# Performance work log

Measured on AMD Instinct MI355X. Metric: run time of the kernel, lower is better.

## Reference

```python
import jax, jax.numpy as jnp
import numpy as np

NUM_RBF = 16
TOP_K = 30
LOWER = 0.0
UPPER = 20.0
MAX_REL = 32  # PositionalEncodings max_relative_feature


def layer_norm(x, g, b, eps=1e-5):
    m = jnp.mean(x, -1, keepdims=True)
    v = jnp.var(x, -1, keepdims=True)
    return (x - m) / jnp.sqrt(v + eps) * g + b


def rbf(D):
    # exp(-((D - mu)/sigma)^2), mu = linspace(LOWER, UPPER, NUM_RBF)
    mu = jnp.linspace(LOWER, UPPER, NUM_RBF)
    sigma = (UPPER - LOWER) / NUM_RBF
    return jnp.exp(-(((D[..., None] - mu) / sigma) ** 2))


def setup_inputs() -> dict:
    key = jax.random.key(0)
    ks = jax.random.split(key, 6)
    B, L, A = 1, 1536, 14
    x = jax.random.normal(ks[0], (B, L, A, 3), jnp.float32) * 5.0
    S = jax.random.randint(ks[1], (B, L), 0, 21)
    mask = jnp.ones((B, L), jnp.float32)
    atom14_mask = jnp.ones((B, L, A), jnp.float32)
    R_idx = jnp.broadcast_to(jnp.arange(L, dtype=jnp.int32), (B, L))
    chain_labels = jnp.zeros((B, L), jnp.int32)
    protein_mpnn_feat = jax.random.normal(ks[2], (B, L, 128), jnp.float32)
    W_pos = jax.random.normal(ks[3], (2 * MAX_REL + 2, 16), jnp.float32) * 0.12
    b_pos = jnp.zeros((16,), jnp.float32)
    W_edge = jax.random.normal(ks[4], (16 + NUM_RBF * 14 * 14, 128), jnp.float32) * 0.018
    gamma_e = jnp.ones((128,), jnp.float32)
    beta_e = jnp.zeros((128,), jnp.float32)
    W_node = jax.random.normal(ks[5], (21 + 128, 128), jnp.float32) * 0.08
    gamma_n = jnp.ones((128,), jnp.float32)
    beta_n = jnp.zeros((128,), jnp.float32)
    return dict(x=x, mask=mask, atom14_mask=atom14_mask,
                protein_mpnn_feat=protein_mpnn_feat,
                W_pos=W_pos, b_pos=b_pos, W_edge=W_edge, gamma_e=gamma_e,
                beta_e=beta_e, W_node=W_node, gamma_n=gamma_n, beta_n=beta_n,
                S=S, R_idx=R_idx, chain_labels=chain_labels)


def reference(x, mask, atom14_mask, protein_mpnn_feat,
              W_pos, b_pos, W_edge, gamma_e, beta_e,
              W_node, gamma_n, beta_n, S, R_idx, chain_labels):
    B, L, A, _ = x.shape  # A = 14
    X_m = atom14_mask * mask[:, :, None]          # [B,L,14]
    Ca = x[:, :, 1]                                # CA_idx = 1

    # ---- _dist: masked pairwise CA distances + kNN topk (smallest) ----
    m2 = mask[:, None, :] * mask[:, :, None]       # [B,L,L]
    dX = Ca[:, None, :, :] - Ca[:, :, None, :]
    D = m2 * jnp.sqrt(jnp.sum(dX ** 2, -1) + 1e-6)
    D_max = jnp.max(D, -1, keepdims=True)
    D_adjust = D + (1.0 - m2) * D_max
    _, E_idx = jax.lax.top_k(-D_adjust, TOP_K)     # [B,L,K] smallest distances

    bidx = jnp.arange(B)[:, None, None]
    # gather neighbor atom coords / masks (all_coords_list == x in atom14 order)
    Xg = x[bidx, E_idx]                            # [B,L,K,14,3]
    Xm_g = X_m[bidx, E_idx]                        # [B,L,K,14]

    # ---- 14x14 pairwise atom RBFs to neighbors, fused/vectorized ----
    # Dp[b,l,k,i,j] = ||x[b,l,i] - x[b,E_idx[b,l,k],j]||
    Dp = jnp.sqrt(jnp.sum((x[:, :, None, :, None, :] - Xg[:, :, :, None, :, :]) ** 2, -1) + 1e-6)
    R = rbf(Dp)                                    # [B,L,K,14,14,16]
    R = R * X_m[:, :, None, :, None, None] * Xm_g[:, :, :, None, :, None]
    # torch loop cats atom_1-major, atom_2, then rbf bins -> same as reshape
    RBF_all = R.reshape(B, L, TOP_K, A * A * NUM_RBF)  # [B,L,K,3136]

    # ---- positional encodings ----
    offset = R_idx[:, :, None] - R_idx[:, None, :]           # [B,L,L]
    offset_g = jnp.take_along_axis(offset, E_idx, axis=2)    # [B,L,K]
    d_chains = (chain_labels[:, :, None] == chain_labels[:, None, :]).astype(jnp.int32)
    E_chains = jnp.take_along_axis(d_chains, E_idx, axis=2)  # [B,L,K]
    d = jnp.clip(offset_g + MAX_REL, 0, 2 * MAX_REL) * E_chains \
        + (1 - E_chains) * (2 * MAX_REL + 1)
    E_pos = jax.nn.one_hot(d, 2 * MAX_REL + 2, dtype=x.dtype) @ W_pos + b_pos

    # ---- edge embedding ----
    E = jnp.concatenate([E_pos, RBF_all], -1) @ W_edge       # [B,L,K,128]
    E = layer_norm(E, gamma_e, beta_e)

    # ---- node embedding ----
    V = jnp.concatenate([jax.nn.one_hot(S, 21, dtype=x.dtype), protein_mpnn_feat], -1) @ W_node
    V = layer_norm(V, gamma_n, beta_n)

    return (V, E, E_idx, x)
```

## Files before the change

### kernel.cpp

```cpp
#include <hip/hip_runtime.h>
#include <hip/hip_bf16.h>
#include <hip/hip_fp16.h>
#include <math.h>

#define LL 1536
#define NA 14
#define TOPK 30
#define KDIM 3152
#define KPAD 3200
#define NCHUNK 50

#define TOPK_BLKS 384
#define CONV_BLKS 100
#define NODE_BLKS 384
#define PREP_BLKS (TOPK_BLKS + CONV_BLKS + NODE_BLKS)

#define EDGE_BLKS 768

typedef __attribute__((ext_vector_type(8))) short bf16x8;
typedef __attribute__((ext_vector_type(4))) float f32x4;

static __device__ __forceinline__ ushort f2bf(float f) {
    union { __hip_bfloat16 h; ushort u; } v;
    v.h = __float2bfloat16(f);
    return v.u;
}

static __device__ __forceinline__ float fexp2(float f) {
    return __builtin_amdgcn_exp2f(f);
}

static __device__ __forceinline__ unsigned cvt_pk_bf16(float lo, float hi) {
    unsigned r;
    asm("v_cvt_pk_bf16_f32 %0, %1, %2" : "=v"(r) : "v"(lo), "v"(hi));
    return r;
}

static __device__ __forceinline__ unsigned long long u64min(
    unsigned long long a, unsigned long long b) { return a < b ? a : b; }

#define ASYNC16(ldsp, gp)                                                     \
    __builtin_amdgcn_global_load_lds(                                         \
        (const __attribute__((address_space(1))) void*)(gp),                  \
        (__attribute__((address_space(3))) void*)(ldsp), 16, 0, 0)

__global__ __launch_bounds__(256) void prep_kernel(
    const float* __restrict__ x, const float* __restrict__ mask,
    const float* __restrict__ feat,
    const float* __restrict__ W_edge, ushort* __restrict__ Wt,
    const float* __restrict__ W_node, const float* __restrict__ gamma_n,
    const float* __restrict__ beta_n, const int* __restrict__ S,
    float* __restrict__ V, float* __restrict__ out_idx, float* __restrict__ out_x)
{
    __shared__ __align__(16) char sm[24576];
    const int blk = blockIdx.x;
    const int tid = threadIdx.x;

    if (blk < TOPK_BLKS) {
        float* ca  = (float*)sm;
        float* msk = (float*)sm + 4608;
        for (int t = tid; t < LL; t += 256) {
            msk[t] = mask[t];
            ca[t * 3 + 0] = x[t * 42 + 3];
            ca[t * 3 + 1] = x[t * 42 + 4];
            ca[t * 3 + 2] = x[t * 42 + 5];
        }
        __syncthreads();

        const int lane = tid & 63;
        const int i = blk * 4 + (tid >> 6);
        const float cix = ca[i * 3 + 0], ciy = ca[i * 3 + 1], ciz = ca[i * 3 + 2];
        const float mi = msk[i];

        float d[24], m2a[24];
        float lmax = 0.f;
        #pragma unroll
        for (int c = 0; c < 24; ++c) {
            int j = lane + c * 64;
            float dx = ca[j * 3 + 0] - cix;
            float dy = ca[j * 3 + 1] - ciy;
            float dz = ca[j * 3 + 2] - ciz;
            float m2 = mi * msk[j];
            float D = m2 * sqrtf(dx * dx + dy * dy + dz * dz + 1e-6f);
            d[c] = D; m2a[c] = m2;
            lmax = fmaxf(lmax, D);
        }
        #pragma unroll
        for (int m = 1; m < 64; m <<= 1) lmax = fmaxf(lmax, __shfl_xor(lmax, m));

        unsigned long long key[24];
        #pragma unroll
        for (int c = 0; c < 24; ++c) {
            float adj = d[c] + (1.f - m2a[c]) * lmax;
            key[c] = ((unsigned long long)__float_as_uint(adj) << 32)
                   | (unsigned)(lane + c * 64);
        }
        for (int t = 0; t < TOPK; ++t) {
            unsigned long long m12[12];
            #pragma unroll
            for (int c = 0; c < 12; ++c) m12[c] = u64min(key[2 * c], key[2 * c + 1]);
            #pragma unroll
            for (int c = 0; c < 6; ++c) m12[c] = u64min(m12[2 * c], m12[2 * c + 1]);
            unsigned long long best = u64min(u64min(m12[0], m12[1]),
                u64min(m12[2], u64min(m12[3], u64min(m12[4], m12[5]))));
            #pragma unroll
            for (int m = 1; m < 64; m <<= 1) best = u64min(best, __shfl_xor(best, m));
            if (lane == 0) out_idx[i * TOPK + t] = (float)(unsigned)(best & 0xffffffffu);
            #pragma unroll
            for (int c = 0; c < 24; ++c) if (key[c] == best) key[c] = ~0ull;
        }
        for (int t = lane; t < 42; t += 64) out_x[i * 42 + t] = x[i * 42 + t];

    } else if (blk < TOPK_BLKS + CONV_BLKS) {
        int cb = blk - TOPK_BLKS;
        int k0 = (cb % 50) * 64, n0 = (cb / 50) * 64;
        float (*tile)[65] = (float (*)[65])sm;
        #pragma unroll
        for (int r = 0; r < 16; ++r) {
            int idx = r * 256 + tid;
            int kl = idx >> 6, nl = idx & 63;
            int k = k0 + kl;
            tile[nl][kl] = (k < KDIM) ? W_edge[k * 128 + n0 + nl] : 0.f;
        }
        __syncthreads();
        #pragma unroll
        for (int r = 0; r < 8; ++r) {
            int idx = r * 256 + tid;
            int nl = idx >> 5, kp = (idx & 31) * 2;
            unsigned pk = cvt_pk_bf16(tile[nl][kp], tile[nl][kp + 1]);
            *(unsigned*)&Wt[(size_t)(n0 + nl) * KPAD + k0 + kp] = pk;
        }

    } else {
        int nb = blk - TOPK_BLKS - CONV_BLKS;
        float* f = (float*)sm;
        const int w = tid >> 6, lane = tid & 63;
        const int i = nb * 4 + w;
        f[w * 128 + lane] = feat[i * 128 + lane];
        f[w * 128 + 64 + lane] = feat[i * 128 + 64 + lane];
        __syncthreads();
        int s = S[i];
        float a0 = W_node[s * 128 + lane];
        float a1 = W_node[s * 128 + 64 + lane];
        #pragma unroll 8
        for (int c = 0; c < 128; ++c) {
            float fc = f[w * 128 + c];
            a0 = fmaf(fc, W_node[(21 + c) * 128 + lane], a0);
            a1 = fmaf(fc, W_node[(21 + c) * 128 + 64 + lane], a1);
        }
        float ss = a0 + a1, qq = a0 * a0 + a1 * a1;
        #pragma unroll
        for (int m = 1; m < 64; m <<= 1) {
            ss += __shfl_xor(ss, m);
            qq += __shfl_xor(qq, m);
        }
        float mean = ss * (1.f / 128.f);
        float var = qq * (1.f / 128.f) - mean * mean;
        float inv = 1.f / sqrtf(var + 1e-5f);
        V[i * 128 + lane]      = (a0 - mean) * inv * gamma_n[lane] + beta_n[lane];
        V[i * 128 + 64 + lane] = (a1 - mean) * inv * gamma_n[64 + lane] + beta_n[64 + lane];
    }
}

__global__ __launch_bounds__(256, 3) void edge_mfma_kernel(
    const float* __restrict__ x, const float* __restrict__ mask,
    const float* __restrict__ a14m, const float* __restrict__ W_pos,
    const float* __restrict__ b_pos, const ushort* __restrict__ Wt,
    const float* __restrict__ gamma, const float* __restrict__ beta,
    const int* __restrict__ R_idx, const int* __restrict__ chain,
    const float* __restrict__ idxf, float* __restrict__ E)
{
    __shared__ __align__(16) char arena[45824];
    ushort* Bs    = (ushort*)arena;
    __half* ddc   = (__half*)(arena + 16384);
    ushort* eposs = (ushort*)(arena + 41984);
    int*    jl    = (int*)(arena + 44032);
    float*  lnS   = (float*)(arena + 44288);
    float*  lnQ   = (float*)(arena + 44800);
    float*  xi    = (float*)(arena + 45312);
    float*  mi    = (float*)(arena + 45664);

    const int i0 = blockIdx.x * 2;
    const int tid = threadIdx.x;
    const int wave = tid >> 6, lane = tid & 63;

    if (tid < 64) {
        int g = tid >> 5, e = tid & 31;
        jl[tid] = (e < TOPK) ? (int)idxf[(i0 + g) * TOPK + e] : 0;
    } else if (tid < 64 + 84) {
        int t = tid - 64; int g = t / 42, c = t - g * 42;
        xi[g * 44 + c] = x[(i0 + g) * 42 + c];
    } else if (tid < 148 + 28) {
        int t = tid - 148; int g = t / 14, a = t - g * 14;
        mi[g * 16 + a] = a14m[(i0 + g) * 14 + a] * mask[i0 + g];
    }
    __syncthreads();

    const int srow = wave * 32 + (lane >> 3);
    const int sseg = (lane & 7) ^ ((lane >> 3) & 7);
    const ushort* gsrc = Wt + (size_t)srow * KPAD + sseg * 8;
    #pragma unroll
    for (int it = 0; it < 4; ++it)
        ASYNC16(Bs + wave * 2048 + it * 512, gsrc + (size_t)it * 8 * KPAD);

    for (int t = tid; t < 64 * 16; t += 256) {
        int row = t >> 4, c = t & 15;
        int e = row & 31, g = row >> 5;
        float v = 0.f;
        if (e < TOPK) {
            int i = i0 + g, j = jl[row];
            int off = R_idx[i] - R_idx[j];
            int ec = (chain[i] == chain[j]) ? 1 : 0;
            int dc = off + 32; dc = dc < 0 ? 0 : (dc > 64 ? 64 : dc);
            int d = ec ? dc : 65;
            v = W_pos[d * 16 + c] + b_pos[c];
        }
        eposs[row * 16 + c] = f2bf(v);
    }

    for (int t = tid; t < 64 * 196; t += 256) {
        int row = t / 196, p = t - row * 196;
        int a1 = p / 14, a2 = p - a1 * 14;
        int g = row >> 5, e = row & 31;
        int j = jl[row];
        const float* xj = &x[j * 42 + a2 * 3];
        float dx = xi[g * 44 + a1 * 3 + 0] - xj[0];
        float dy = xi[g * 44 + a1 * 3 + 1] - xj[1];
        float dz = xi[g * 44 + a1 * 3 + 2] - xj[2];
        float dd = sqrtf(dx * dx + dy * dy + dz * dz + 1e-6f);
        float cj_ = (e < TOPK) ? a14m[j * 14 + a2] * mask[j] : 0.f;
        float coef = mi[g * 16 + a1] * cj_;
        ddc[row * 200 + p] = __float2half((coef > 0.5f) ? fminf(dd, 27.f) : 40.f);
    }
    __syncthreads();

    const int l16 = lane & 15, lk = lane >> 4;
    const int mh = wave >> 1, nh = wave & 1;
    const int r0 = 8 * (lk & 1);
    const float mu0 = (float)r0 * 1.33333333f;
    float wc[7];
    #pragma unroll
    for (int j = 1; j < 8; ++j)
        wc[j - 1] = __expf(-1.13777778f * (float)(2 * (r0 + j) - 1));

    int boff[2][4];
    #pragma unroll
    for (int ks = 0; ks < 2; ++ks)
        #pragma unroll
        for (int nf = 0; nf < 4; ++nf) {
            int n = nh * 64 + nf * 16 + l16;
            boff[ks][nf] = n * 64 + ((((ks << 2) | lk) ^ (n & 7)) << 3);
        }
    int doff[2], eoff[2];
    #pragma unroll
    for (int mf = 0; mf < 2; ++mf) {
        int row = mh * 32 + mf * 16 + l16;
        doff[mf] = row * 200;
        eoff[mf] = row * 16 + r0;
    }

    f32x4 acc[2][4] = {};

    for (int ch = 0; ch < NCHUNK; ++ch) {
        bf16x8 bfr[2][4];
        #pragma unroll
        for (int ks = 0; ks < 2; ++ks)
            #pragma unroll
            for (int nf = 0; nf < 4; ++nf)
                bfr[ks][nf] = *(const bf16x8*)&Bs[boff[ks][nf]];
        __syncthreads();
        if (ch + 1 < NCHUNK) {
            #pragma unroll
            for (int it = 0; it < 4; ++it)
                ASYNC16(Bs + wave * 2048 + it * 512,
                        gsrc + (size_t)it * 8 * KPAD + (ch + 1) * 64);
        }
        bf16x8 af[2][2];
        #pragma unroll
        for (int ks = 0; ks < 2; ++ks) {
            const int p = 4 * ch + 2 * ks + (lk >> 1) - 1;
            #pragma unroll
            for (int mf = 0; mf < 2; ++mf) {
                if (p < 0) {
                    af[ks][mf] = *(const bf16x8*)&eposs[eoff[mf]];
                } else if (p < 196) {
                    float dd = __half2float(ddc[doff[mf] + p]);
                    float w = fexp2(dd * 2.46219921f);
                    float s = dd - mu0;
                    float ev[8];
                    ev[0] = fexp2(s * s * -0.92332483f);
                    #pragma unroll
                    for (int j = 1; j < 8; ++j) ev[j] = ev[j - 1] * w * wc[j - 1];
                    union { unsigned u[4]; bf16x8 v; } o;
                    #pragma unroll
                    for (int j = 0; j < 4; ++j)
                        o.u[j] = cvt_pk_bf16(ev[2 * j], ev[2 * j + 1]);
                    af[ks][mf] = o.v;
                } else {
                    af[ks][mf] = (bf16x8){0, 0, 0, 0, 0, 0, 0, 0};
                }
            }
        }
        #pragma unroll
        for (int ks = 0; ks < 2; ++ks)
            #pragma unroll
            for (int mf = 0; mf < 2; ++mf)
                #pragma unroll
                for (int nf = 0; nf < 4; ++nf)
                    acc[mf][nf] = __builtin_amdgcn_mfma_f32_16x16x32_bf16(
                        af[ks][mf], bfr[ks][nf], acc[mf][nf], 0, 0, 0);
        __syncthreads();
    }

    #pragma unroll
    for (int mf = 0; mf < 2; ++mf)
        #pragma unroll
        for (int reg = 0; reg < 4; ++reg) {
            float s = acc[mf][0][reg] + acc[mf][1][reg] + acc[mf][2][reg] + acc[mf][3][reg];
            float q = acc[mf][0][reg] * acc[mf][0][reg] + acc[mf][1][reg] * acc[mf][1][reg]
                    + acc[mf][2][reg] * acc[mf][2][reg] + acc[mf][3][reg] * acc[mf][3][reg];
            #pragma unroll
            for (int m = 1; m < 16; m <<= 1) {
                s += __shfl_xor(s, m);
                q += __shfl_xor(q, m);
            }
            if (l16 == 0) {
                int row = mh * 32 + mf * 16 + lk * 4 + reg;
                lnS[row * 2 + nh] = s;
                lnQ[row * 2 + nh] = q;
            }
        }
    __syncthreads();

    float gl[4], bl[4];
    #pragma unroll
    for (int nf = 0; nf < 4; ++nf) {
        int col = nh * 64 + nf * 16 + l16;
        gl[nf] = gamma[col];
        bl[nf] = beta[col];
    }
    #pragma unroll
    for (int mf = 0; mf < 2; ++mf)
        #pragma unroll
        for (int reg = 0; reg < 4; ++reg) {
            int r = mh * 32 + mf * 16 + lk * 4 + reg;
            int e = r & 31, g = r >> 5;
            if (e < TOPK) {
                float s = lnS[r * 2 + 0] + lnS[r * 2 + 1];
                float q = lnQ[r * 2 + 0] + lnQ[r * 2 + 1];
                float mean = s * (1.f / 128.f);
                float var = q * (1.f / 128.f) - mean * mean;
                float inv = 1.f / sqrtf(var + 1e-5f);
                float* dst = &E[((size_t)((i0 + g) * TOPK + e)) * 128];
                #pragma unroll
                for (int nf = 0; nf < 4; ++nf) {
                    int col = nh * 64 + nf * 16 + l16;
                    dst[col] = (acc[mf][nf][reg] - mean) * inv * gl[nf] + bl[nf];
                }
            }
        }
}

extern "C" void kernel_launch(void* const* d_in, const int* in_sizes, int n_in,
                              void* d_out, int out_size, void* d_ws, size_t ws_size,
                              hipStream_t stream)
{
    const float* x       = (const float*)d_in[0];
    const float* mask    = (const float*)d_in[1];
    const float* a14m    = (const float*)d_in[2];
    const float* feat    = (const float*)d_in[3];
    const float* W_pos   = (const float*)d_in[4];
    const float* b_pos   = (const float*)d_in[5];
    const float* W_edge  = (const float*)d_in[6];
    const float* gamma_e = (const float*)d_in[7];
    const float* beta_e  = (const float*)d_in[8];
    const float* W_node  = (const float*)d_in[9];
    const float* gamma_n = (const float*)d_in[10];
    const float* beta_n  = (const float*)d_in[11];
    const int*   S       = (const int*)d_in[12];
    const int*   R_idx   = (const int*)d_in[13];
    const int*   chain   = (const int*)d_in[14];

    float* out     = (float*)d_out;
    float* V       = out;
    float* E       = out + 196608;
    float* out_idx = out + 196608 + 5898240;
    float* out_x   = out_idx + 46080;

    ushort* Wt = (ushort*)d_ws;

    prep_kernel<<<PREP_BLKS, 256, 0, stream>>>(
        x, mask, feat, W_edge, Wt, W_node, gamma_n, beta_n, S, V, out_idx, out_x);
    edge_mfma_kernel<<<EDGE_BLKS, 256, 0, stream>>>(
        x, mask, a14m, W_pos, b_pos, Wt, gamma_e, beta_e, R_idx, chain,
        out_idx, E);
}
```

Measured before the change: 121.3 us.

## Restructure edge GEMM: LDS double-buffered RBF A-tiles, register-prefetched W from global

```diff
diff --git a/kernel.cpp b/kernel.cpp
--- a/kernel.cpp
+++ b/kernel.cpp
@@ -20,12 +20,6 @@
 typedef __attribute__((ext_vector_type(8))) short bf16x8;
 typedef __attribute__((ext_vector_type(4))) float f32x4;
 
-static __device__ __forceinline__ ushort f2bf(float f) {
-    union { __hip_bfloat16 h; ushort u; } v;
-    v.h = __float2bfloat16(f);
-    return v.u;
-}
-
 static __device__ __forceinline__ float fexp2(float f) {
     return __builtin_amdgcn_exp2f(f);
 }
@@ -39,10 +33,30 @@
 static __device__ __forceinline__ unsigned long long u64min(
     unsigned long long a, unsigned long long b) { return a < b ? a : b; }
 
-#define ASYNC16(ldsp, gp)                                                     \
-    __builtin_amdgcn_global_load_lds(                                         \
-        (const __attribute__((address_space(1))) void*)(gp),                  \
-        (__attribute__((address_space(3))) void*)(ldsp), 16, 0, 0)
+static __device__ __forceinline__ void build_rbf(
+    ushort* dst, float4 xi4, float4 xj4,
+    const float (&cA)[7], const float (&cB)[7])
+{
+    float dx = xi4.x - xj4.x, dy = xi4.y - xj4.y, dz = xi4.z - xj4.z;
+    float dd = sqrtf(dx * dx + dy * dy + dz * dz + 1e-6f);
+    dd = fminf(dd, 27.f);
+    float coef = xi4.w * xj4.w;
+    float w = fexp2(dd * 2.46219921f);
+    float ev[16];
+    float s8 = dd - 10.66666667f;
+    ev[0] = fexp2(-0.92332483f * dd * dd) * coef;
+    ev[8] = fexp2(-0.92332483f * s8 * s8) * coef;
+    #pragma unroll
+    for (int j = 1; j <= 7; ++j) {
+        ev[j]     = ev[j - 1]     * w * cA[j - 1];
+        ev[8 + j] = ev[8 + j - 1] * w * cB[j - 1];
+    }
+    union { unsigned u[8]; uint4 q[2]; } o;
+    #pragma unroll
+    for (int c = 0; c < 8; ++c) o.u[c] = cvt_pk_bf16(ev[2 * c], ev[2 * c + 1]);
+    *(uint4*)&dst[0] = o.q[0];
+    *(uint4*)&dst[8] = o.q[1];
+}
 
 __global__ __launch_bounds__(256) void prep_kernel(
     const float* __restrict__ x, const float* __restrict__ mask,
@@ -170,15 +184,12 @@
     const int* __restrict__ R_idx, const int* __restrict__ chain,
     const float* __restrict__ idxf, float* __restrict__ E)
 {
-    __shared__ __align__(16) char arena[45824];
-    ushort* Bs    = (ushort*)arena;
-    __half* ddc   = (__half*)(arena + 16384);
-    ushort* eposs = (ushort*)(arena + 41984);
-    int*    jl    = (int*)(arena + 44032);
-    float*  lnS   = (float*)(arena + 44288);
-    float*  lnQ   = (float*)(arena + 44800);
-    float*  xi    = (float*)(arena + 45312);
-    float*  mi    = (float*)(arena + 45664);
+    __shared__ __align__(16) ushort As[2][64][72];
+    __shared__ __align__(16) float4 xjr[64][14];
+    __shared__ __align__(16) float4 xir[2][14];
+    __shared__ int   jl[64];
+    __shared__ float lnS[64][2];
+    __shared__ float lnQ[64][2];
 
     const int i0 = blockIdx.x * 2;
     const int tid = threadIdx.x;
@@ -187,130 +198,130 @@
     if (tid < 64) {
         int g = tid >> 5, e = tid & 31;
         jl[tid] = (e < TOPK) ? (int)idxf[(i0 + g) * TOPK + e] : 0;
-    } else if (tid < 64 + 84) {
-        int t = tid - 64; int g = t / 42, c = t - g * 42;
-        xi[g * 44 + c] = x[(i0 + g) * 42 + c];
-    } else if (tid < 148 + 28) {
-        int t = tid - 148; int g = t / 14, a = t - g * 14;
-        mi[g * 16 + a] = a14m[(i0 + g) * 14 + a] * mask[i0 + g];
+    } else if (tid < 64 + 28) {
+        int t = tid - 64, g = t / 14, a = t - g * 14;
+        const float* xp = &x[(i0 + g) * 42 + a * 3];
+        xir[g][a] = make_float4(xp[0], xp[1], xp[2],
+                                a14m[(i0 + g) * 14 + a] * mask[i0 + g]);
     }
     __syncthreads();
 
-    const int srow = wave * 32 + (lane >> 3);
-    const int sseg = (lane & 7) ^ ((lane >> 3) & 7);
-    const ushort* gsrc = Wt + (size_t)srow * KPAD + sseg * 8;
-    #pragma unroll
-    for (int it = 0; it < 4; ++it)
-        ASYNC16(Bs + wave * 2048 + it * 512, gsrc + (size_t)it * 8 * KPAD);
-
-    for (int t = tid; t < 64 * 16; t += 256) {
-        int row = t >> 4, c = t & 15;
-        int e = row & 31, g = row >> 5;
-        float v = 0.f;
-        if (e < TOPK) {
-            int i = i0 + g, j = jl[row];
+    for (int t = tid; t < 64 * 14; t += 256) {
+        int row = t / 14, a = t - row * 14;
+        int e = row & 31, j = jl[row];
+        const float* xp = &x[j * 42 + a * 3];
+        float mj = (e < TOPK) ? a14m[j * 14 + a] * mask[j] : 0.f;
+        xjr[row][a] = make_float4(xp[0], xp[1], xp[2], mj);
+    }
+    __syncthreads();
+
+    const int l16 = lane & 15, lk = lane >> 4, lk8 = lk * 8;
+    const int mh = wave >> 1, nh = wave & 1;
+    const int arow0 = mh * 32 + l16, arow1 = arow0 + 16;
+    const int row_b = tid >> 2, slot = tid & 3;
+    const int gb = row_b >> 5, eb = row_b & 31;
+
+    float cA[7], cB[7];
+    #pragma unroll
+    for (int j = 1; j <= 7; ++j) {
+        cA[j - 1] = __expf(-1.13777778f * (float)(2 * j - 1));
+        cB[j - 1] = __expf(-1.13777778f * (float)(2 * (j + 8) - 1));
+    }
+
+    if (slot == 0) {
+        float v[16];
+        if (eb < TOPK) {
+            int i = i0 + gb, j = jl[row_b];
             int off = R_idx[i] - R_idx[j];
             int ec = (chain[i] == chain[j]) ? 1 : 0;
             int dc = off + 32; dc = dc < 0 ? 0 : (dc > 64 ? 64 : dc);
             int d = ec ? dc : 65;
-            v = W_pos[d * 16 + c] + b_pos[c];
-        }
-        eposs[row * 16 + c] = f2bf(v);
-    }
-
-    for (int t = tid; t < 64 * 196; t += 256) {
-        int row = t / 196, p = t - row * 196;
-        int a1 = p / 14, a2 = p - a1 * 14;
-        int g = row >> 5, e = row & 31;
-        int j = jl[row];
-        const float* xj = &x[j * 42 + a2 * 3];
-        float dx = xi[g * 44 + a1 * 3 + 0] - xj[0];
-        float dy = xi[g * 44 + a1 * 3 + 1] - xj[1];
-        float dz = xi[g * 44 + a1 * 3 + 2] - xj[2];
-        float dd = sqrtf(dx * dx + dy * dy + dz * dz + 1e-6f);
-        float cj_ = (e < TOPK) ? a14m[j * 14 + a2] * mask[j] : 0.f;
-        float coef = mi[g * 16 + a1] * cj_;
-        ddc[row * 200 + p] = __float2half((coef > 0.5f) ? fminf(dd, 27.f) : 40.f);
-    }
+            #pragma unroll
+            for (int c = 0; c < 16; ++c) v[c] = W_pos[d * 16 + c] + b_pos[c];
+        } else {
+            #pragma unroll
+            for (int c = 0; c < 16; ++c) v[c] = 0.f;
+        }
+        union { unsigned u[8]; uint4 q[2]; } o;
+        #pragma unroll
+        for (int c = 0; c < 8; ++c) o.u[c] = cvt_pk_bf16(v[2 * c], v[2 * c + 1]);
+        *(uint4*)&As[0][row_b][0] = o.q[0];
+        *(uint4*)&As[0][row_b][8] = o.q[1];
+    } else {
+        build_rbf(&As[0][row_b][slot * 16], xir[gb][slot - 1],
+                  xjr[row_b][slot - 1], cA, cB);
+    }
+
+    const ushort* bp0 = Wt + (size_t)(nh * 64 +  0 + l16) * KPAD + lk8;
+    const ushort* bp1 = Wt + (size_t)(nh * 64 + 16 + l16) * KPAD + lk8;
+    const ushort* bp2 = Wt + (size_t)(nh * 64 + 32 + l16) * KPAD + lk8;
+    const ushort* bp3 = Wt + (size_t)(nh * 64 + 48 + l16) * KPAD + lk8;
+
+    bf16x8 Ba[2][4], Bb[2][4];
+    Ba[0][0] = *(const bf16x8*)(bp0);      Ba[1][0] = *(const bf16x8*)(bp0 + 32);
+    Ba[0][1] = *(const bf16x8*)(bp1);      Ba[1][1] = *(const bf16x8*)(bp1 + 32);
+    Ba[0][2] = *(const bf16x8*)(bp2);      Ba[1][2] = *(const bf16x8*)(bp2 + 32);
+    Ba[0][3] = *(const bf16x8*)(bp3);      Ba[1][3] = *(const bf16x8*)(bp3 + 32);
+
+    int p = slot + 3, a1 = 0, a2 = slot + 3;
+    f32x4 acc[2][4] = {};
+
     __syncthreads();
 
-    const int l16 = lane & 15, lk = lane >> 4;
-    const int mh = wave >> 1, nh = wave & 1;
-    const int r0 = 8 * (lk & 1);
-    const float mu0 = (float)r0 * 1.33333333f;
-    float wc[7];
-    #pragma unroll
-    for (int j = 1; j < 8; ++j)
-        wc[j - 1] = __expf(-1.13777778f * (float)(2 * (r0 + j) - 1));
-
-    int boff[2][4];
-    #pragma unroll
-    for (int ks = 0; ks < 2; ++ks)
-        #pragma unroll
-        for (int nf = 0; nf < 4; ++nf) {
-            int n = nh * 64 + nf * 16 + l16;
-            boff[ks][nf] = n * 64 + ((((ks << 2) | lk) ^ (n & 7)) << 3);
-        }
-    int doff[2], eoff[2];
-    #pragma unroll
-    for (int mf = 0; mf < 2; ++mf) {
-        int row = mh * 32 + mf * 16 + l16;
-        doff[mf] = row * 200;
-        eoff[mf] = row * 16 + r0;
-    }
-
-    f32x4 acc[2][4] = {};
-
-    for (int ch = 0; ch < NCHUNK; ++ch) {
-        bf16x8 bfr[2][4];
-        #pragma unroll
-        for (int ks = 0; ks < 2; ++ks)
-            #pragma unroll
-            for (int nf = 0; nf < 4; ++nf)
-                bfr[ks][nf] = *(const bf16x8*)&Bs[boff[ks][nf]];
-        __syncthreads();
-        if (ch + 1 < NCHUNK) {
-            #pragma unroll
-            for (int it = 0; it < 4; ++it)
-                ASYNC16(Bs + wave * 2048 + it * 512,
-                        gsrc + (size_t)it * 8 * KPAD + (ch + 1) * 64);
-        }
-        bf16x8 af[2][2];
-        #pragma unroll
-        for (int ks = 0; ks < 2; ++ks) {
-            const int p = 4 * ch + 2 * ks + (lk >> 1) - 1;
-            #pragma unroll
-            for (int mf = 0; mf < 2; ++mf) {
-                if (p < 0) {
-                    af[ks][mf] = *(const bf16x8*)&eposs[eoff[mf]];
-                } else if (p < 196) {
-                    float dd = __half2float(ddc[doff[mf] + p]);
-                    float w = fexp2(dd * 2.46219921f);
-                    float s = dd - mu0;
-                    float ev[8];
-                    ev[0] = fexp2(s * s * -0.92332483f);
-                    #pragma unroll
-                    for (int j = 1; j < 8; ++j) ev[j] = ev[j - 1] * w * wc[j - 1];
-                    union { unsigned u[4]; bf16x8 v; } o;
-                    #pragma unroll
-                    for (int j = 0; j < 4; ++j)
-                        o.u[j] = cvt_pk_bf16(ev[2 * j], ev[2 * j + 1]);
-                    af[ks][mf] = o.v;
-                } else {
-                    af[ks][mf] = (bf16x8){0, 0, 0, 0, 0, 0, 0, 0};
-                }
-            }
-        }
-        #pragma unroll
-        for (int ks = 0; ks < 2; ++ks)
-            #pragma unroll
-            for (int mf = 0; mf < 2; ++mf)
-                #pragma unroll
-                for (int nf = 0; nf < 4; ++nf)
-                    acc[mf][nf] = __builtin_amdgcn_mfma_f32_16x16x32_bf16(
-                        af[ks][mf], bfr[ks][nf], acc[mf][nf], 0, 0, 0);
-        __syncthreads();
-    }
+#define STEP(CH, RD, BC, BN)                                                   \
+    do {                                                                       \
+        if ((CH) + 1 < NCHUNK) {                                               \
+            const size_t koff = (size_t)((CH) + 1) * 64;                       \
+            BN[0][0] = *(const bf16x8*)(bp0 + koff);                           \
+            BN[1][0] = *(const bf16x8*)(bp0 + koff + 32);                      \
+            BN[0][1] = *(const bf16x8*)(bp1 + koff);                           \
+            BN[1][1] = *(const bf16x8*)(bp1 + koff + 32);                      \
+            BN[0][2] = *(const bf16x8*)(bp2 + koff);                           \
+            BN[1][2] = *(const bf16x8*)(bp2 + koff + 32);                      \
+            BN[0][3] = *(const bf16x8*)(bp3 + koff);                           \
+            BN[1][3] = *(const bf16x8*)(bp3 + koff + 32);                      \
+        }                                                                      \
+        {                                                                      \
+            bf16x8 af0k0 = *(const bf16x8*)&As[RD][arow0][lk8];                \
+            bf16x8 af1k0 = *(const bf16x8*)&As[RD][arow1][lk8];                \
+            bf16x8 af0k1 = *(const bf16x8*)&As[RD][arow0][32 + lk8];           \
+            bf16x8 af1k1 = *(const bf16x8*)&As[RD][arow1][32 + lk8];           \
+            acc[0][0] = __builtin_amdgcn_mfma_f32_16x16x32_bf16(af0k0, BC[0][0], acc[0][0], 0, 0, 0); \
+            acc[0][1] = __builtin_amdgcn_mfma_f32_16x16x32_bf16(af0k0, BC[0][1], acc[0][1], 0, 0, 0); \
+            acc[0][2] = __builtin_amdgcn_mfma_f32_16x16x32_bf16(af0k0, BC[0][2], acc[0][2], 0, 0, 0); \
+            acc[0][3] = __builtin_amdgcn_mfma_f32_16x16x32_bf16(af0k0, BC[0][3], acc[0][3], 0, 0, 0); \
+            acc[1][0] = __builtin_amdgcn_mfma_f32_16x16x32_bf16(af1k0, BC[0][0], acc[1][0], 0, 0, 0); \
+            acc[1][1] = __builtin_amdgcn_mfma_f32_16x16x32_bf16(af1k0, BC[0][1], acc[1][1], 0, 0, 0); \
+            acc[1][2] = __builtin_amdgcn_mfma_f32_16x16x32_bf16(af1k0, BC[0][2], acc[1][2], 0, 0, 0); \
+            acc[1][3] = __builtin_amdgcn_mfma_f32_16x16x32_bf16(af1k0, BC[0][3], acc[1][3], 0, 0, 0); \
+            acc[0][0] = __builtin_amdgcn_mfma_f32_16x16x32_bf16(af0k1, BC[1][0], acc[0][0], 0, 0, 0); \
+            acc[0][1] = __builtin_amdgcn_mfma_f32_16x16x32_bf16(af0k1, BC[1][1], acc[0][1], 0, 0, 0); \
+            acc[0][2] = __builtin_amdgcn_mfma_f32_16x16x32_bf16(af0k1, BC[1][2], acc[0][2], 0, 0, 0); \
+            acc[0][3] = __builtin_amdgcn_mfma_f32_16x16x32_bf16(af0k1, BC[1][3], acc[0][3], 0, 0, 0); \
+            acc[1][0] = __builtin_amdgcn_mfma_f32_16x16x32_bf16(af1k1, BC[1][0], acc[1][0], 0, 0, 0); \
+            acc[1][1] = __builtin_amdgcn_mfma_f32_16x16x32_bf16(af1k1, BC[1][1], acc[1][1], 0, 0, 0); \
+            acc[1][2] = __builtin_amdgcn_mfma_f32_16x16x32_bf16(af1k1, BC[1][2], acc[1][2], 0, 0, 0); \
+            acc[1][3] = __builtin_amdgcn_mfma_f32_16x16x32_bf16(af1k1, BC[1][3], acc[1][3], 0, 0, 0); \
+        }                                                                      \
+        if ((CH) < NCHUNK - 1) {                                               \
+            if (p <= 195) {                                                    \
+                build_rbf(&As[1 - (RD)][row_b][slot * 16], xir[gb][a1],        \
+                          xjr[row_b][a2], cA, cB);                             \
+            } else {                                                           \
+                uint4 z = {0u, 0u, 0u, 0u};                                    \
+                *(uint4*)&As[1 - (RD)][row_b][slot * 16] = z;                  \
+                *(uint4*)&As[1 - (RD)][row_b][slot * 16 + 8] = z;              \
+            }                                                                  \
+            p += 4; a2 += 4; if (a2 >= 14) { a2 -= 14; ++a1; }                 \
+        }                                                                      \
+        __syncthreads();                                                       \
+    } while (0)
+
+    for (int ch = 0; ch < NCHUNK; ch += 2) {
+        STEP(ch, 0, Ba, Bb);
+        STEP(ch + 1, 1, Bb, Ba);
+    }
+#undef STEP
 
     #pragma unroll
     for (int mf = 0; mf < 2; ++mf)
@@ -326,8 +337,8 @@
             }
             if (l16 == 0) {
                 int row = mh * 32 + mf * 16 + lk * 4 + reg;
-                lnS[row * 2 + nh] = s;
-                lnQ[row * 2 + nh] = q;
+                lnS[row][nh] = s;
+                lnQ[row][nh] = q;
             }
         }
     __syncthreads();
@@ -346,8 +357,8 @@
             int r = mh * 32 + mf * 16 + lk * 4 + reg;
             int e = r & 31, g = r >> 5;
             if (e < TOPK) {
-                float s = lnS[r * 2 + 0] + lnS[r * 2 + 1];
-                float q = lnQ[r * 2 + 0] + lnQ[r * 2 + 1];
+                float s = lnS[r][0] + lnS[r][1];
+                float q = lnQ[r][0] + lnQ[r][1];
                 float mean = s * (1.f / 128.f);
                 float var = q * (1.f / 128.f) - mean * mean;
                 float inv = 1.f / sqrtf(var + 1e-5f);
```

After: 184.2 us. 51.8% more time.
